# Performance work log

Measured on AMD Instinct MI355X. Metric: run time of the kernel, lower is better.

Reference implementation:

```python
import jax, jax.numpy as jnp
import numpy as np

N_NODES = 100000
N_EDGES = 3200000
IN_DIM, HID, OUT = 512, 256, 64


def setup_inputs() -> dict:
    key = jax.random.key(0)
    k1, k2, k3, k4, k5, k6 = jax.random.split(key, 6)
    x = jax.random.normal(k1, (N_NODES, IN_DIM), dtype=jnp.float32)
    edge_src = jax.random.randint(k2, (N_EDGES,), 0, N_NODES, dtype=jnp.int32)
    edge_dst = jax.random.randint(k3, (N_EDGES,), 0, N_NODES, dtype=jnp.int32)
    edge_val = jax.random.uniform(k4, (N_EDGES,), dtype=jnp.float32)
    # glorot init as in the original `glorot([input_dim, output_dim])`
    w1 = jax.random.normal(k5, (IN_DIM, HID), dtype=jnp.float32) * np.sqrt(2.0 / (IN_DIM + HID))
    w2 = jax.random.normal(k6, (HID, OUT), dtype=jnp.float32) * np.sqrt(2.0 / (HID + OUT))
    return {"x": x, "edge_src": edge_src, "edge_dst": edge_dst,
            "edge_val": edge_val, "w1": w1, "w2": w2}


def _spmm(edge_src, edge_dst, edge_val, dense):
    # support @ dense : out[i] = sum_j A[i,j] * dense[j], A given as COO edges
    msgs = edge_val[:, None] * dense[edge_dst]            # [E, D] gather
    return jax.ops.segment_sum(msgs, edge_src, num_segments=N_NODES)  # scatter-add


def reference(x, edge_src, edge_dst, edge_val, w1, w2):
    # Layer 1: pre_sup = X @ W1 ; support = A @ pre_sup ; relu (no bias)
    h = jax.nn.relu(_spmm(edge_src, edge_dst, edge_val, x @ w1))  # [N, HID]
    # Layer 2: identity activation
    logits = _spmm(edge_src, edge_dst, edge_val, h @ w2)          # [N, OUT]
    return logits
```

## Files before the change

kernel.cpp:

```cpp
#include <hip/hip_runtime.h>

#define NN 100000
#define NE 3200000
#define IN_DIM 512
#define HID 256
#define OUTD 64
#define NB 196
#define CAP 20480
#define EPB 3125

typedef _Float16 f16x8 __attribute__((ext_vector_type(8)));
typedef float f32x4 __attribute__((ext_vector_type(4)));

__device__ __forceinline__ void async_copy16(void* lds, const void* g) {
    __builtin_amdgcn_global_load_lds(
        (const __attribute__((address_space(1))) void*)g,
        (__attribute__((address_space(3))) void*)lds, 16, 0, 0);
}

__device__ __forceinline__ float b2f(int w, int b) {
    return (float)((w << (24 - 8 * b)) >> 24);
}


__global__ void init_cursor_kernel(int* __restrict__ cursor) {
    int t = threadIdx.x;
    if (t < NB) cursor[t] = t * CAP;
}

__global__ __launch_bounds__(256) void bin_kernel(const int* __restrict__ src,
                                                  const int* __restrict__ dst,
                                                  const float* __restrict__ val,
                                                  int* __restrict__ cursor,
                                                  int* __restrict__ srcs_tmp,
                                                  int2* __restrict__ pairs_tmp,
                                                  int E) {
    __shared__ int s_src[EPB];
    __shared__ int s_dst[EPB];
    __shared__ int s_val[EPB];
    __shared__ int hist[NB];
    __shared__ int base[NB];
    const int t = threadIdx.x;
    const int lo = blockIdx.x * EPB;
    const int cnt = min(E - lo, EPB);
    for (int i = t; i < NB; i += 256) hist[i] = 0;
    for (int i = t; i < cnt; i += 256) {
        s_src[i] = src[lo + i];
        s_dst[i] = dst[lo + i];
        s_val[i] = __float_as_int(val[lo + i]);
    }
    __syncthreads();
    for (int i = t; i < cnt; i += 256) atomicAdd(&hist[s_src[i] >> 9], 1);
    __syncthreads();
    for (int i = t; i < NB; i += 256) {
        base[i] = atomicAdd(&cursor[i], hist[i]);
        hist[i] = 0;
    }
    __syncthreads();
    for (int i = t; i < cnt; i += 256) {
        int s = s_src[i];
        int b = s >> 9;
        int l = atomicAdd(&hist[b], 1);
        int pos = base[b] + l;
        srcs_tmp[pos] = s;
        pairs_tmp[pos] = make_int2(s_dst[i], s_val[i]);
    }
}

__global__ void bucket_scan_kernel(const int* __restrict__ cursor,
                                   int* __restrict__ bbase, int* __restrict__ offs) {
    __shared__ int sz[NB];
    int t = threadIdx.x;
    if (t < NB) sz[t] = cursor[t] - t * CAP;
    __syncthreads();
    if (t == 0) {
        int acc = 0;
        for (int i = 0; i < NB; ++i) { bbase[i] = acc; acc += sz[i]; }
        bbase[NB] = acc;
        offs[NN] = acc;
    }
}

#define CSR_LDS 18432
__global__ __launch_bounds__(1024) void csr_kernel(const int* __restrict__ cursor,
                                                   const int* __restrict__ bbase,
                                                   const int* __restrict__ srcs_tmp,
                                                   const int2* __restrict__ pairs_tmp,
                                                   const float* __restrict__ scales,
                                                   int* __restrict__ offs,
                                                   int2* __restrict__ pairs) {
    __shared__ int ssrc[CSR_LDS];
    __shared__ int cnt[512];
    __shared__ int wsum[8];
    const int b = blockIdx.x;
    const int t = threadIdx.x;
    const int s0 = b << 9;
    const int base = bbase[b];
    const int n_b = cursor[b] - b * CAP;
    const int tlo = b * CAP;
    if (t < 512) cnt[t] = 0;
    __syncthreads();
    for (int i = t; i < n_b; i += 1024) {
        int s = srcs_tmp[tlo + i] - s0;
        ssrc[i] = s;
        atomicAdd(&cnt[s], 1);
    }
    __syncthreads();
    int my = 0, incl = 0;
    if (t < 512) {
        my = cnt[t];
        incl = my;
        #pragma unroll
        for (int d = 1; d < 64; d <<= 1) {
            int y = __shfl_up(incl, d);
            if ((t & 63) >= d) incl += y;
        }
        if ((t & 63) == 63) wsum[t >> 6] = incl;
    }
    __syncthreads();
    if (t == 0) {
        int acc = 0;
        #pragma unroll
        for (int i = 0; i < 8; ++i) { int v = wsum[i]; wsum[i] = acc; acc += v; }
    }
    __syncthreads();
    if (t < 512) {
        int excl = base + incl - my + wsum[t >> 6];
        int s = s0 + t;
        if (s < NN) offs[s] = excl;
        cnt[t] = excl;
    }
    __syncthreads();
    for (int i = t; i < n_b; i += 1024) {
        int s = ssrc[i];
        int p = atomicAdd(&cnt[s], 1);
        int2 pv = pairs_tmp[tlo + i];
        pv.y = __float_as_int(__int_as_float(pv.y) * scales[pv.x]);
        pairs[p] = pv;
    }
}


__global__ void transpose_cast2(const float* __restrict__ w1, const float* __restrict__ w2,
                                _Float16* __restrict__ w1t, _Float16* __restrict__ w2t) {
    int idx = blockIdx.x * blockDim.x + threadIdx.x;
    if (idx < IN_DIM * HID) {
        int k = idx / HID, n = idx % HID;
        w1t[(size_t)n * IN_DIM + k] = (_Float16)w1[idx];
    } else if (idx < IN_DIM * HID + HID * OUTD) {
        int j = idx - IN_DIM * HID;
        int k = j / OUTD, n = j % OUTD;
        w2t[(size_t)n * HID + k] = (_Float16)w2[j];
    }
}


__global__ __launch_bounds__(256) void gemm1_f32a(const float* __restrict__ A,
                                                  const _Float16* __restrict__ Bt,
                                                  signed char* __restrict__ qC,
                                                  float* __restrict__ scales,
                                                  int M) {
    __shared__ float    As[128 * 32];
    __shared__ _Float16 Bs[256 * 32];
    __shared__ float    rmaxl[2][128];
    const int tid  = threadIdx.x;
    const int lane = tid & 63;
    const int wave = tid >> 6;
    const int wm = wave >> 1, wn = wave & 1;
    const int m0 = blockIdx.x * 128;

    f32x4 acc[4][8];
    #pragma unroll
    for (int i = 0; i < 4; ++i)
        #pragma unroll
        for (int j = 0; j < 8; ++j) acc[i][j] = (f32x4){0.f, 0.f, 0.f, 0.f};

    for (int k0 = 0; k0 < IN_DIM; k0 += 32) {
        #pragma unroll
        for (int it = 0; it < 4; ++it) {
            int i = it * 256 + tid;
            int r = i >> 3;
            int cp = i & 7;
            int cl = cp ^ (r & 7);
            int gr = m0 + r; if (gr >= M) gr = M - 1;
            async_copy16((char*)As + i * 16, A + (size_t)gr * IN_DIM + k0 + cl * 4);
        }
        #pragma unroll
        for (int it = 0; it < 4; ++it) {
            int i = it * 256 + tid;
            int r = i >> 2;
            int cp = i & 3;
            int cl = cp ^ (r & 3);
            async_copy16((char*)Bs + i * 16, Bt + (size_t)r * IN_DIM + k0 + cl * 8);
        }
        __syncthreads();

        const int kc = lane >> 4;
        f16x8 af[4];
        #pragma unroll
        for (int m = 0; m < 4; ++m) {
            int r = wm * 64 + m * 16 + (lane & 15);
            int p0 = (2 * kc) ^ (r & 7);
            int p1 = (2 * kc + 1) ^ (r & 7);
            f32x4 c0 = *(const f32x4*)((const char*)As + r * 128 + p0 * 16);
            f32x4 c1 = *(const f32x4*)((const char*)As + r * 128 + p1 * 16);
            f16x8 v = { (_Float16)c0[0], (_Float16)c0[1], (_Float16)c0[2], (_Float16)c0[3],
                        (_Float16)c1[0], (_Float16)c1[1], (_Float16)c1[2], (_Float16)c1[3] };
            af[m] = v;
        }
        f16x8 bf[8];
        #pragma unroll
        for (int n = 0; n < 8; ++n) {
            int r = wn * 128 + n * 16 + (lane & 15);
            bf[n] = *(const f16x8*)((const char*)Bs + r * 64 + ((kc ^ (r & 3)) * 16));
        }
        #pragma unroll
        for (int m = 0; m < 4; ++m)
            #pragma unroll
            for (int n = 0; n < 8; ++n)
                acc[m][n] = __builtin_amdgcn_mfma_f32_16x16x32_f16(af[m], bf[n], acc[m][n], 0, 0, 0);
        __syncthreads();
    }

    #pragma unroll
    for (int m = 0; m < 4; ++m)
        #pragma unroll
        for (int r = 0; r < 4; ++r) {
            float mm = 0.f;
            #pragma unroll
            for (int n = 0; n < 8; ++n) mm = fmaxf(mm, fabsf(acc[m][n][r]));
            #pragma unroll
            for (int d = 1; d < 16; d <<= 1) mm = fmaxf(mm, __shfl_xor(mm, d));
            if ((lane & 15) == 0)
                rmaxl[wn][wm * 64 + m * 16 + (lane >> 4) * 4 + r] = mm;
        }
    __syncthreads();
    #pragma unroll
    for (int m = 0; m < 4; ++m)
        #pragma unroll
        for (int r = 0; r < 4; ++r) {
            int lrow = wm * 64 + m * 16 + (lane >> 4) * 4 + r;
            int row = m0 + lrow;
            float full = fmaxf(fmaxf(rmaxl[0][lrow], rmaxl[1][lrow]), 1e-12f);
            float inv = 127.0f / full;
            if (row < M) {
                #pragma unroll
                for (int n = 0; n < 8; ++n) {
                    int col = wn * 128 + n * 16 + (lane & 15);
                    qC[(size_t)row * HID + col] = (signed char)__float2int_rn(acc[m][n][r] * inv);
                }
                if (wn == 0 && (lane & 15) == 0) scales[row] = full * (1.0f / 127.0f);
            }
        }
}


__global__ __launch_bounds__(256) void spmm_relu_mm2(const int* __restrict__ offs,
                                                     const int2* __restrict__ pairs,
                                                     const signed char* __restrict__ qpre,
                                                     const float* __restrict__ scales,
                                                     const _Float16* __restrict__ w2t,
                                                     signed char* __restrict__ qh2,
                                                     float* __restrict__ ratio2, int n) {
    __shared__ _Float16 hl[32][17][8];
    __shared__ float rmax2[4][16];
    const int tid  = threadIdx.x;
    const int lane = tid & 63;
    const int wid  = tid >> 6;
    const int par  = lane >> 4;
    const int fl   = lane & 15;
    const int nbase = blockIdx.x * 16;
    const signed char* qbase = qpre + fl * 16;

    #pragma unroll 1
    for (int i = 0; i < 4; ++i) {
        const int node = nbase + wid * 4 + i;
        const int beg = offs[node], end = offs[node + 1];
        float a[16] = {};
        int k = beg;
        for (; k + 16 <= end; k += 16) {
            int2 pr[4];
            #pragma unroll
            for (int j = 0; j < 4; ++j) pr[j] = pairs[k + 4 * j + par];
            int4 qv[4];
            #pragma unroll
            for (int j = 0; j < 4; ++j)
                qv[j] = *(const int4*)(qbase + (size_t)pr[j].x * HID);
            #pragma unroll
            for (int j = 0; j < 4; ++j) {
                float m = __int_as_float(pr[j].y);
                int w0 = qv[j].x, w1 = qv[j].y, w2 = qv[j].z, w3 = qv[j].w;
                #pragma unroll
                for (int b = 0; b < 4; ++b) {
                    a[b]      = fmaf(m, b2f(w0, b), a[b]);
                    a[4 + b]  = fmaf(m, b2f(w1, b), a[4 + b]);
                    a[8 + b]  = fmaf(m, b2f(w2, b), a[8 + b]);
                    a[12 + b] = fmaf(m, b2f(w3, b), a[12 + b]);
                }
            }
        }
        if (k < end) {
            int2 pr[4];
            float m_[4];
            #pragma unroll
            for (int j = 0; j < 4; ++j) {
                int idx = k + 4 * j + par;
                int cidx = idx < end ? idx : end - 1;
                pr[j] = pairs[cidx];
                m_[j] = idx < end ? __int_as_float(pr[j].y) : 0.f;
            }
            int4 qv[4];
            #pragma unroll
            for (int j = 0; j < 4; ++j)
                qv[j] = *(const int4*)(qbase + (size_t)pr[j].x * HID);
            #pragma unroll
            for (int j = 0; j < 4; ++j) {
                float m = m_[j];
                int w0 = qv[j].x, w1 = qv[j].y, w2 = qv[j].z, w3 = qv[j].w;
                #pragma unroll
                for (int b = 0; b < 4; ++b) {
                    a[b]      = fmaf(m, b2f(w0, b), a[b]);
                    a[4 + b]  = fmaf(m, b2f(w1, b), a[4 + b]);
                    a[8 + b]  = fmaf(m, b2f(w2, b), a[8 + b]);
                    a[12 + b] = fmaf(m, b2f(w3, b), a[12 + b]);
                }
            }
        }
        #pragma unroll
        for (int q = 0; q < 16; ++q) {
            a[q] += __shfl_xor(a[q], 16);
            a[q] += __shfl_xor(a[q], 32);
        }
        if (par == 0) {
            f16x8 o0, o1;
            #pragma unroll
            for (int q = 0; q < 8; ++q) {
                o0[q] = (_Float16)fmaxf(a[q], 0.f);
                o1[q] = (_Float16)fmaxf(a[8 + q], 0.f);
            }
            *(f16x8*)&hl[2 * fl][wid * 4 + i][0]     = o0;
            *(f16x8*)&hl[2 * fl + 1][wid * 4 + i][0] = o1;
        }
    }
    __syncthreads();

    const int r  = lane & 15;
    const int kc = lane >> 4;
    f32x4 acc = (f32x4){0.f, 0.f, 0.f, 0.f};
    #pragma unroll
    for (int kk = 0; kk < 8; ++kk) {
        f16x8 af = *(const f16x8*)&hl[kk * 4 + kc][r][0];
        f16x8 bf = *(const f16x8*)(w2t + (size_t)(wid * 16 + r) * HID + kk * 32 + kc * 8);
        acc = __builtin_amdgcn_mfma_f32_16x16x32_f16(af, bf, acc, 0, 0, 0);
    }
    float mxv[4];
    #pragma unroll
    for (int j = 0; j < 4; ++j) {
        float mm = fabsf(acc[j]);
        #pragma unroll
        for (int d = 1; d < 16; d <<= 1) mm = fmaxf(mm, __shfl_xor(mm, d));
        mxv[j] = mm;
    }
    if (r == 0) {
        #pragma unroll
        for (int j = 0; j < 4; ++j) rmax2[wid][kc * 4 + j] = mxv[j];
    }
    __syncthreads();
    #pragma unroll
    for (int j = 0; j < 4; ++j) {
        int ln = kc * 4 + j;
        int node = nbase + ln;
        float full = fmaxf(fmaxf(fmaxf(rmax2[0][ln], rmax2[1][ln]),
                                 fmaxf(rmax2[2][ln], rmax2[3][ln])), 1e-12f);
        qh2[(size_t)node * OUTD + wid * 16 + r] =
            (signed char)__float2int_rn(acc[j] * (127.0f / full));
        if (wid == 0 && r == 0)
            ratio2[node] = full * (1.0f / 127.0f) / scales[node];
    }
}


__global__ __launch_bounds__(256) void spmm64_q(const int* __restrict__ offs,
                                                const int2* __restrict__ pairs,
                                                const signed char* __restrict__ qh2,
                                                const float* __restrict__ ratio2,
                                                float* __restrict__ out, int n) {
    int node = blockIdx.x * 4 + (threadIdx.x >> 6);
    if (node >= n) return;
    int lane = threadIdx.x & 63;
    int par = lane >> 3;
    int fl  = lane & 7;
    int beg = offs[node], end = offs[node + 1];
    const signed char* qbase = qh2 + fl * 8;
    float a[8] = {};
    int k = beg;
    for (; k + 32 <= end; k += 32) {
        int2 pr[4];
        #pragma unroll
        for (int j = 0; j < 4; ++j) pr[j] = pairs[k + 8 * j + par];
        int2 qv[4];
        #pragma unroll
        for (int j = 0; j < 4; ++j)
            qv[j] = *(const int2*)(qbase + (size_t)pr[j].x * OUTD);
        float m_[4];
        #pragma unroll
        for (int j = 0; j < 4; ++j)
            m_[j] = __int_as_float(pr[j].y) * ratio2[pr[j].x];
        #pragma unroll
        for (int j = 0; j < 4; ++j) {
            int lo = qv[j].x, hi = qv[j].y;
            a[0] = fmaf(m_[j], b2f(lo, 0), a[0]);
            a[1] = fmaf(m_[j], b2f(lo, 1), a[1]);
            a[2] = fmaf(m_[j], b2f(lo, 2), a[2]);
            a[3] = fmaf(m_[j], b2f(lo, 3), a[3]);
            a[4] = fmaf(m_[j], b2f(hi, 0), a[4]);
            a[5] = fmaf(m_[j], b2f(hi, 1), a[5]);
            a[6] = fmaf(m_[j], b2f(hi, 2), a[6]);
            a[7] = fmaf(m_[j], b2f(hi, 3), a[7]);
        }
    }
    if (k < end) {
        int2 pr[4];
        float m_[4];
        #pragma unroll
        for (int j = 0; j < 4; ++j) {
            int idx = k + 8 * j + par;
            int cidx = idx < end ? idx : end - 1;
            pr[j] = pairs[cidx];
            m_[j] = idx < end ? __int_as_float(pr[j].y) * ratio2[pr[j].x] : 0.f;
        }
        int2 qv[4];
        #pragma unroll
        for (int j = 0; j < 4; ++j)
            qv[j] = *(const int2*)(qbase + (size_t)pr[j].x * OUTD);
        #pragma unroll
        for (int j = 0; j < 4; ++j) {
            int lo = qv[j].x, hi = qv[j].y;
            a[0] = fmaf(m_[j], b2f(lo, 0), a[0]);
            a[1] = fmaf(m_[j], b2f(lo, 1), a[1]);
            a[2] = fmaf(m_[j], b2f(lo, 2), a[2]);
            a[3] = fmaf(m_[j], b2f(lo, 3), a[3]);
            a[4] = fmaf(m_[j], b2f(hi, 0), a[4]);
            a[5] = fmaf(m_[j], b2f(hi, 1), a[5]);
            a[6] = fmaf(m_[j], b2f(hi, 2), a[6]);
            a[7] = fmaf(m_[j], b2f(hi, 3), a[7]);
        }
    }
    #pragma unroll
    for (int q = 0; q < 8; ++q) {
        a[q] += __shfl_xor(a[q], 8);
        a[q] += __shfl_xor(a[q], 16);
        a[q] += __shfl_xor(a[q], 32);
    }
    if (par == 0) {
        float4 o0 = make_float4(a[0], a[1], a[2], a[3]);
        float4 o1 = make_float4(a[4], a[5], a[6], a[7]);
        *(float4*)(out + (size_t)node * OUTD + fl * 8)     = o0;
        *(float4*)(out + (size_t)node * OUTD + fl * 8 + 4) = o1;
    }
}


extern "C" void kernel_launch(void* const* d_in, const int* in_sizes, int n_in,
                              void* d_out, int out_size, void* d_ws, size_t ws_size,
                              hipStream_t stream) {
    const float* x    = (const float*)d_in[0];
    const int*   esrc = (const int*)d_in[1];
    const int*   edst = (const int*)d_in[2];
    const float* eval = (const float*)d_in[3];
    const float* w1   = (const float*)d_in[4];
    const float* w2   = (const float*)d_in[5];
    float* out = (float*)d_out;

    char* ws = (char*)d_ws;
    signed char* qpre    = (signed char*)(ws + 0);
    signed char* qh2     = (signed char*)(ws + 25600000);
    float*       scales  = (float*)(ws + 32000000);
    float*       ratio2  = (float*)(ws + 32400000);
    int2*        pairs   = (int2*)(ws + 32800000);
    int2*        pairs_t = (int2*)(ws + 58400000);
    int*         srcs_t  = (int*)(ws + 90512640);
    int*         cursor  = (int*)(ws + 106568960);
    int*         bbase   = (int*)(ws + 106569984);
    int*         offs    = (int*)(ws + 106571008);
    _Float16*    w1t     = (_Float16*)(ws + 106971136);
    _Float16*    w2t     = (_Float16*)(ws + 107233280);

    init_cursor_kernel<<<1, 256, 0, stream>>>(cursor);
    bin_kernel<<<1024, 256, 0, stream>>>(esrc, edst, eval, cursor, srcs_t, pairs_t, NE);
    bucket_scan_kernel<<<1, 256, 0, stream>>>(cursor, bbase, offs);

    transpose_cast2<<<(IN_DIM * HID + HID * OUTD + 255) / 256, 256, 0, stream>>>(w1, w2, w1t, w2t);
    gemm1_f32a<<<(NN + 127) / 128, 256, 0, stream>>>(x, w1t, qpre, scales, NN);

    csr_kernel<<<NB, 1024, 0, stream>>>(cursor, bbase, srcs_t, pairs_t, scales, offs, pairs);

    spmm_relu_mm2<<<NN / 16, 256, 0, stream>>>(offs, pairs, qpre, scales, w2t, qh2, ratio2, NN);

    spmm64_q<<<(NN + 3) / 4, 256, 0, stream>>>(offs, pairs, qh2, ratio2, out, NN);
}
```

Before: 447.9 us.

## Fold ratio2 into edge weights and widen layer-2 SpMM loads to 16 bytes

Adds a separate pass that multiplies each edge value by ratio2 of its neighbour and writes the result into a reused workspace buffer. The second SpMM then no longer does the per-edge ratio2 gather. That SpMM also switches from 8-byte to 16-byte row loads, using 4 lanes per row and 16 parallel edges, with one more shuffle stage in the reduction. The LDS padding in spmm_relu_mm2 changes from 17 to 18. In exchange there is an extra kernel launch and an extra pass that reads and writes 3.2M pairs (about 51MB of traffic).

```diff
diff --git a/kernel.cpp b/kernel.cpp
--- a/kernel.cpp
+++ b/kernel.cpp
@@ -262,7 +262,7 @@
                                                      const _Float16* __restrict__ w2t,
                                                      signed char* __restrict__ qh2,
                                                      float* __restrict__ ratio2, int n) {
-    __shared__ _Float16 hl[32][17][8];
+    __shared__ _Float16 hl[32][18][8];
     __shared__ float rmax2[4][16];
     const int tid  = threadIdx.x;
     const int lane = tid & 63;
@@ -380,83 +380,93 @@
 }
 
 
+__global__ __launch_bounds__(256) void scale_fold(const int2* __restrict__ pairs,
+                                                  const float* __restrict__ ratio2,
+                                                  int2* __restrict__ pairs2, int E) {
+    int e = blockIdx.x * blockDim.x + threadIdx.x;
+    if (e < E) {
+        int2 pv = pairs[e];
+        pv.y = __float_as_int(__int_as_float(pv.y) * ratio2[pv.x]);
+        pairs2[e] = pv;
+    }
+}
+
+
 __global__ __launch_bounds__(256) void spmm64_q(const int* __restrict__ offs,
-                                                const int2* __restrict__ pairs,
+                                                const int2* __restrict__ pairs2,
                                                 const signed char* __restrict__ qh2,
-                                                const float* __restrict__ ratio2,
                                                 float* __restrict__ out, int n) {
     int node = blockIdx.x * 4 + (threadIdx.x >> 6);
     if (node >= n) return;
     int lane = threadIdx.x & 63;
-    int par = lane >> 3;
-    int fl  = lane & 7;
+    int par = lane >> 2;
+    int fl  = lane & 3;
     int beg = offs[node], end = offs[node + 1];
-    const signed char* qbase = qh2 + fl * 8;
-    float a[8] = {};
+    const signed char* qbase = qh2 + fl * 16;
+    float a[16] = {};
     int k = beg;
     for (; k + 32 <= end; k += 32) {
-        int2 pr[4];
-        #pragma unroll
-        for (int j = 0; j < 4; ++j) pr[j] = pairs[k + 8 * j + par];
-        int2 qv[4];
-        #pragma unroll
-        for (int j = 0; j < 4; ++j)
-            qv[j] = *(const int2*)(qbase + (size_t)pr[j].x * OUTD);
-        float m_[4];
-        #pragma unroll
-        for (int j = 0; j < 4; ++j)
-            m_[j] = __int_as_float(pr[j].y) * ratio2[pr[j].x];
-        #pragma unroll
-        for (int j = 0; j < 4; ++j) {
-            int lo = qv[j].x, hi = qv[j].y;
-            a[0] = fmaf(m_[j], b2f(lo, 0), a[0]);
-            a[1] = fmaf(m_[j], b2f(lo, 1), a[1]);
-            a[2] = fmaf(m_[j], b2f(lo, 2), a[2]);
-            a[3] = fmaf(m_[j], b2f(lo, 3), a[3]);
-            a[4] = fmaf(m_[j], b2f(hi, 0), a[4]);
-            a[5] = fmaf(m_[j], b2f(hi, 1), a[5]);
-            a[6] = fmaf(m_[j], b2f(hi, 2), a[6]);
-            a[7] = fmaf(m_[j], b2f(hi, 3), a[7]);
+        int2 pr[2];
+        #pragma unroll
+        for (int j = 0; j < 2; ++j) pr[j] = pairs2[k + 16 * j + par];
+        int4 qv[2];
+        #pragma unroll
+        for (int j = 0; j < 2; ++j)
+            qv[j] = *(const int4*)(qbase + (size_t)pr[j].x * OUTD);
+        #pragma unroll
+        for (int j = 0; j < 2; ++j) {
+            float m = __int_as_float(pr[j].y);
+            int w0 = qv[j].x, w1 = qv[j].y, w2 = qv[j].z, w3 = qv[j].w;
+            #pragma unroll
+            for (int b = 0; b < 4; ++b) {
+                a[b]      = fmaf(m, b2f(w0, b), a[b]);
+                a[4 + b]  = fmaf(m, b2f(w1, b), a[4 + b]);
+                a[8 + b]  = fmaf(m, b2f(w2, b), a[8 + b]);
+                a[12 + b] = fmaf(m, b2f(w3, b), a[12 + b]);
+            }
         }
     }
     if (k < end) {
-        int2 pr[4];
-        float m_[4];
-        #pragma unroll
-        for (int j = 0; j < 4; ++j) {
-            int idx = k + 8 * j + par;
+        int2 pr[2];
+        float m_[2];
+        #pragma unroll
+        for (int j = 0; j < 2; ++j) {
+            int idx = k + 16 * j + par;
             int cidx = idx < end ? idx : end - 1;
-            pr[j] = pairs[cidx];
-            m_[j] = idx < end ? __int_as_float(pr[j].y) * ratio2[pr[j].x] : 0.f;
-        }
-        int2 qv[4];
-        #pragma unroll
-        for (int j = 0; j < 4; ++j)
-            qv[j] = *(const int2*)(qbase + (size_t)pr[j].x * OUTD);
-        #pragma unroll
-        for (int j = 0; j < 4; ++j) {
-            int lo = qv[j].x, hi = qv[j].y;
-            a[0] = fmaf(m_[j], b2f(lo, 0), a[0]);
-            a[1] = fmaf(m_[j], b2f(lo, 1), a[1]);
-            a[2] = fmaf(m_[j], b2f(lo, 2), a[2]);
-            a[3] = fmaf(m_[j], b2f(lo, 3), a[3]);
-            a[4] = fmaf(m_[j], b2f(hi, 0), a[4]);
-            a[5] = fmaf(m_[j], b2f(hi, 1), a[5]);
-            a[6] = fmaf(m_[j], b2f(hi, 2), a[6]);
-            a[7] = fmaf(m_[j], b2f(hi, 3), a[7]);
-        }
-    }
-    #pragma unroll
-    for (int q = 0; q < 8; ++q) {
+            pr[j] = pairs2[cidx];
+            m_[j] = idx < end ? __int_as_float(pr[j].y) : 0.f;
+        }
+        int4 qv[2];
+        #pragma unroll
+        for (int j = 0; j < 2; ++j)
+            qv[j] = *(const int4*)(qbase + (size_t)pr[j].x * OUTD);
+        #pragma unroll
+        for (int j = 0; j < 2; ++j) {
+            float m = m_[j];
+            int w0 = qv[j].x, w1 = qv[j].y, w2 = qv[j].z, w3 = qv[j].w;
+            #pragma unroll
+            for (int b = 0; b < 4; ++b) {
+                a[b]      = fmaf(m, b2f(w0, b), a[b]);
+                a[4 + b]  = fmaf(m, b2f(w1, b), a[4 + b]);
+                a[8 + b]  = fmaf(m, b2f(w2, b), a[8 + b]);
+                a[12 + b] = fmaf(m, b2f(w3, b), a[12 + b]);
+            }
+        }
+    }
+    #pragma unroll
+    for (int q = 0; q < 16; ++q) {
+        a[q] += __shfl_xor(a[q], 4);
         a[q] += __shfl_xor(a[q], 8);
         a[q] += __shfl_xor(a[q], 16);
         a[q] += __shfl_xor(a[q], 32);
     }
     if (par == 0) {
-        float4 o0 = make_float4(a[0], a[1], a[2], a[3]);
-        float4 o1 = make_float4(a[4], a[5], a[6], a[7]);
-        *(float4*)(out + (size_t)node * OUTD + fl * 8)     = o0;
-        *(float4*)(out + (size_t)node * OUTD + fl * 8 + 4) = o1;
+        float* ob = out + (size_t)node * OUTD + fl * 16;
+        #pragma unroll
+        for (int c = 0; c < 4; ++c) {
+            float4 o = make_float4(a[4 * c], a[4 * c + 1], a[4 * c + 2], a[4 * c + 3]);
+            *(float4*)(ob + 4 * c) = o;
+        }
     }
 }
 
@@ -485,6 +495,7 @@
     int*         offs    = (int*)(ws + 106571008);
     _Float16*    w1t     = (_Float16*)(ws + 106971136);
     _Float16*    w2t     = (_Float16*)(ws + 107233280);
+    int2*        pairs2  = pairs_t;
 
     init_cursor_kernel<<<1, 256, 0, stream>>>(cursor);
     bin_kernel<<<1024, 256, 0, stream>>>(esrc, edst, eval, cursor, srcs_t, pairs_t, NE);
@@ -497,5 +508,7 @@
 
     spmm_relu_mm2<<<NN / 16, 256, 0, stream>>>(offs, pairs, qpre, scales, w2t, qh2, ratio2, NN);
 
-    spmm64_q<<<(NN + 3) / 4, 256, 0, stream>>>(offs, pairs, qh2, ratio2, out, NN);
-}
+    scale_fold<<<(NE + 255) / 256, 256, 0, stream>>>(pairs, ratio2, pairs2, NE);
+
+    spmm64_q<<<(NN + 3) / 4, 256, 0, stream>>>(offs, pairs2, qh2, out, NN);
+}
```

Measured after the change: 467.1 us. 4.3% more time.
